# Kernel optimization log

Measured on AMD Instinct MI355X. Metric: run time of the kernel, lower is better.

The kernel has to match this reference:

```python
import jax, jax.numpy as jnp
import numpy as np

B = 8192
N_LAYERS = 2
NUM_PATCHES = 196  # 14*14
PATCH_OUT = 4
NUM_CLASSES = 10
IMG = 28


def setup_inputs() -> dict:
    key = jax.random.key(0)
    ks = jax.random.split(key, 5)
    x = jax.random.normal(ks[0], (B, 1, IMG, IMG), dtype=jnp.float32)
    ansatz_params = jax.random.normal(ks[1], (N_LAYERS, 4), dtype=jnp.float32)
    Wc = jax.random.normal(ks[2], (NUM_CLASSES, NUM_PATCHES * PATCH_OUT), dtype=jnp.float32) * 0.02
    bc = jnp.zeros((NUM_CLASSES,), jnp.float32)
    Wr = jax.random.normal(ks[3], (IMG * IMG, NUM_PATCHES * PATCH_OUT), dtype=jnp.float32) * 0.02
    br = jnp.zeros((IMG * IMG,), jnp.float32)
    return {"x": x, "ansatz_params": ansatz_params, "Wc": Wc, "bc": bc, "Wr": Wr, "br": br}


def _ry(state, theta, wire):
    # state: (N,2,2,2,2) real (RY and CNOT are real matrices).
    # RY(t) = [[cos(t/2), -sin(t/2)], [sin(t/2), cos(t/2)]]
    ax = wire + 1
    a0 = jnp.take(state, 0, axis=ax)
    a1 = jnp.take(state, 1, axis=ax)
    h = jnp.asarray(theta) * 0.5
    c, s = jnp.cos(h), jnp.sin(h)
    if c.ndim == 1:  # per-sample angle (N,)
        c = c[:, None, None, None]
        s = s[:, None, None, None]
    return jnp.stack([c * a0 - s * a1, s * a0 + c * a1], axis=ax)


def _cnot(state, ctrl, tgt):
    cax, tax = ctrl + 1, tgt + 1
    s0 = jnp.take(state, 0, axis=cax)
    s1 = jnp.take(state, 1, axis=cax)
    tax2 = tax - 1 if tax > cax else tax  # axis shift after removing ctrl axis
    s1 = jnp.flip(s1, axis=tax2)
    return jnp.stack([s0, s1], axis=cax)


def _simulate(patches_flat, params):
    # patches_flat: (N,4) encode angles; params: (L,4)
    N = patches_flat.shape[0]
    state = jnp.zeros((N, 2, 2, 2, 2), patches_flat.dtype).at[:, 0, 0, 0, 0].set(1.0)
    for w in range(4):
        state = _ry(state, patches_flat[:, w], w)
    for l in range(params.shape[0]):
        for w in range(4):
            state = _ry(state, params[l, w], w)
        for c, t in ((0, 1), (1, 2), (2, 3), (3, 0)):
            state = _cnot(state, c, t)
    p = state * state  # probabilities (real amplitudes)
    feats = jnp.stack(
        [jnp.sum(jnp.take(p, 0, axis=w + 1) - jnp.take(p, 1, axis=w + 1), axis=(1, 2, 3)) for w in range(4)],
        axis=-1,
    )  # (N,4) PauliZ expectations
    return feats


def reference(x, ansatz_params, Wc, bc, Wr, br):
    Bn = x.shape[0]
    # unfold(2,2,2).unfold(3,2,2) -> (B,1,14,14,2,2) -> (B,196,4)
    patches = x.reshape(Bn, 1, 14, 2, 14, 2).transpose(0, 1, 2, 4, 3, 5).reshape(Bn, NUM_PATCHES, 4)
    patches = patches / jnp.max(patches)
    feats = _simulate(patches.reshape(-1, 4), ansatz_params)  # (B*196, 4)
    flat = feats.reshape(Bn, NUM_PATCHES * PATCH_OUT)
    logits = flat @ Wc.T + bc
    recon = (flat @ Wr.T + br).reshape(Bn, 1, IMG, IMG)
    return jax.nn.log_softmax(logits, axis=-1), recon
```

## Files before the change

kernel.cpp:

```cpp
#include <hip/hip_runtime.h>
#include <hip/hip_bf16.h>

#define B_SZ   8192
#define NPATCH 196
#define FEAT   784
#define IMGPX  784
#define NCLS   10
#define NALL   794

typedef __attribute__((ext_vector_type(8))) short bf16x8;
typedef __attribute__((ext_vector_type(4))) float fx4;

__device__ inline unsigned f2ord(float f){
    unsigned u = __float_as_uint(f);
    return (u & 0x80000000u) ? ~u : (u | 0x80000000u);
}
__device__ inline float ord2f(unsigned u){
    return (u & 0x80000000u) ? __uint_as_float(u & 0x7FFFFFFFu)
                             : __uint_as_float(~u);
}
__device__ inline unsigned short f2bf(float f){
    union { __hip_bfloat16 h; unsigned short u; } cv;
    cv.h = __float2bfloat16(f);
    return cv.u;
}

__global__ __launch_bounds__(256) void k_max(const float* __restrict__ x,
                                             unsigned* __restrict__ maxslot){
    const int n4 = (B_SZ * IMGPX) / 4;
    float m = -3.0e38f;
    for (int i = blockIdx.x * 256 + threadIdx.x; i < n4; i += gridDim.x * 256){
        float4 v = ((const float4*)x)[i];
        m = fmaxf(m, fmaxf(fmaxf(v.x, v.y), fmaxf(v.z, v.w)));
    }
    #pragma unroll
    for (int off = 32; off > 0; off >>= 1)
        m = fmaxf(m, __shfl_down(m, off, 64));
    __shared__ float sm[4];
    int lane = threadIdx.x & 63, wv = threadIdx.x >> 6;
    if (lane == 0) sm[wv] = m;
    __syncthreads();
    if (threadIdx.x == 0){
        m = fmaxf(fmaxf(sm[0], sm[1]), fmaxf(sm[2], sm[3]));
        atomicMax(maxslot, f2ord(m));
    }
}

__global__ __launch_bounds__(256) void k_prep(const float* __restrict__ Wr,
                                              const float* __restrict__ Wc,
                                              const float* __restrict__ ansatz,
                                              unsigned short* __restrict__ Wall,
                                              float* __restrict__ trig){
    int t = blockIdx.x * 256 + threadIdx.x;
    if (blockIdx.x == 0 && threadIdx.x < 8){
        float p = ansatz[threadIdx.x];
        trig[threadIdx.x]     = cosf(0.5f * p);
        trig[8 + threadIdx.x] = sinf(0.5f * p);
    }
    const int nWr4  = (IMGPX * FEAT) / 4;
    const int nAll4 = (NALL  * FEAT) / 4;
    if (t < nAll4){
        float4 v = (t < nWr4) ? ((const float4*)Wr)[t]
                              : ((const float4*)Wc)[t - nWr4];
        ushort4 o;
        o.x = f2bf(v.x); o.y = f2bf(v.y); o.z = f2bf(v.z); o.w = f2bf(v.w);
        ((ushort4*)Wall)[t] = o;
    }
}

__global__ __launch_bounds__(256) void k_sim(const float* __restrict__ x,
                                             const unsigned* __restrict__ maxslot,
                                             const float* __restrict__ trig,
                                             unsigned short* __restrict__ flatb){
    int idx = blockIdx.x * 256 + threadIdx.x;
    if (idx >= B_SZ * NPATCH) return;
    int b  = idx / NPATCH;
    int p  = idx - b * NPATCH;
    int pi = p / 14;
    int pj = p - pi * 14;
    const float* base = x + b * IMGPX + pi * 2 * 28 + pj * 2;
    float2 r0 = *(const float2*)(base);
    float2 r1 = *(const float2*)(base + 28);
    float inv = 1.0f / ord2f(*maxslot);
    float th[4] = { r0.x * inv, r0.y * inv, r1.x * inv, r1.y * inv };
    float cw[4], sw[4];
    #pragma unroll
    for (int w = 0; w < 4; ++w) __sincosf(0.5f * th[w], &sw[w], &cw[w]);

    float a[16];
    a[0] = cw[0]; a[8] = sw[0];
    #pragma unroll
    for (int s = 0; s < 16; s += 8){ a[s + 4] = a[s] * sw[1]; a[s] *= cw[1]; }
    #pragma unroll
    for (int s = 0; s < 16; s += 4){ a[s + 2] = a[s] * sw[2]; a[s] *= cw[2]; }
    #pragma unroll
    for (int s = 0; s < 16; s += 2){ a[s + 1] = a[s] * sw[3]; a[s] *= cw[3]; }

    #pragma unroll
    for (int l = 0; l < 2; ++l){
        #pragma unroll
        for (int w = 0; w < 4; ++w){
            float cc = trig[l * 4 + w], ss = trig[8 + l * 4 + w];
            int msk = 8 >> w;
            #pragma unroll
            for (int st = 0; st < 16; ++st){
                if (!(st & msk)){
                    int s1 = st | msk;
                    float a0 = a[st], a1 = a[s1];
                    a[st] = cc * a0 - ss * a1;
                    a[s1] = ss * a0 + cc * a1;
                }
            }
        }
        #pragma unroll
        for (int ci = 0; ci < 4; ++ci){
            int cb = 8 >> ci;
            int tb = 8 >> ((ci + 1) & 3);
            #pragma unroll
            for (int st = 0; st < 16; ++st){
                if ((st & cb) && !(st & tb)){
                    int s1 = st | tb;
                    float tmp = a[st]; a[st] = a[s1]; a[s1] = tmp;
                }
            }
        }
    }
    float f0 = 0, f1 = 0, f2 = 0, f3 = 0;
    #pragma unroll
    for (int st = 0; st < 16; ++st){
        float pp = a[st] * a[st];
        f0 += (st & 8) ? -pp : pp;
        f1 += (st & 4) ? -pp : pp;
        f2 += (st & 2) ? -pp : pp;
        f3 += (st & 1) ? -pp : pp;
    }
    ushort4 o; o.x = f2bf(f0); o.y = f2bf(f1); o.z = f2bf(f2); o.w = f2bf(f3);
    ((ushort4*)flatb)[idx] = o;
}

__global__ __launch_bounds__(256) void k_gemm(const unsigned short* __restrict__ Aflat,
                                              const unsigned short* __restrict__ Wall,
                                              const float* __restrict__ br,
                                              const float* __restrict__ bc,
                                              float* __restrict__ recon,
                                              float* __restrict__ logits){
    __shared__ unsigned short As[64][40];
    __shared__ unsigned short Bs[64][40];
    const int t    = threadIdx.x;
    const int bm   = blockIdx.x, bn = blockIdx.y;
    const int lane = t & 63, wv = t >> 6;
    const int r    = lane & 15, q = lane >> 4;
    const int mb   = (wv >> 1) * 32, nb = (wv & 1) * 32;
    const int ldr  = t >> 2, kc = (t & 3) * 8;
    const int gm   = bm * 64 + ldr;
    const int gn   = bn * 64 + ldr;
    const bool bval = gn < NALL;

    fx4 acc[2][2] = {};

    for (int k0 = 0; k0 < FEAT; k0 += 32){
        int kk  = k0 + kc;
        bool kin = kk < FEAT;
        float4 av = {0, 0, 0, 0}, bv = {0, 0, 0, 0};
        if (kin)         av = *(const float4*)(Aflat + (size_t)gm * FEAT + kk);
        if (kin && bval) bv = *(const float4*)(Wall  + (size_t)gn * FEAT + kk);
        *(float4*)(&As[ldr][kc]) = av;
        *(float4*)(&Bs[ldr][kc]) = bv;
        __syncthreads();
        bf16x8 a0 = *(const bf16x8*)(&As[mb +      r][q * 8]);
        bf16x8 a1 = *(const bf16x8*)(&As[mb + 16 + r][q * 8]);
        bf16x8 b0 = *(const bf16x8*)(&Bs[nb +      r][q * 8]);
        bf16x8 b1 = *(const bf16x8*)(&Bs[nb + 16 + r][q * 8]);
        acc[0][0] = __builtin_amdgcn_mfma_f32_16x16x32_bf16(a0, b0, acc[0][0], 0, 0, 0);
        acc[0][1] = __builtin_amdgcn_mfma_f32_16x16x32_bf16(a0, b1, acc[0][1], 0, 0, 0);
        acc[1][0] = __builtin_amdgcn_mfma_f32_16x16x32_bf16(a1, b0, acc[1][0], 0, 0, 0);
        acc[1][1] = __builtin_amdgcn_mfma_f32_16x16x32_bf16(a1, b1, acc[1][1], 0, 0, 0);
        __syncthreads();
    }
    #pragma unroll
    for (int i = 0; i < 2; ++i)
        #pragma unroll
        for (int j = 0; j < 2; ++j)
            #pragma unroll
            for (int v = 0; v < 4; ++v){
                int m = bm * 64 + mb + i * 16 + q * 4 + v;
                int n = bn * 64 + nb + j * 16 + r;
                float val = acc[i][j][v];
                if (n < IMGPX)      recon[(size_t)m * IMGPX + n] = val + br[n];
                else if (n < NALL)  logits[m * NCLS + (n - IMGPX)] = val + bc[n - IMGPX];
            }
}

__global__ __launch_bounds__(256) void k_softmax(const float* __restrict__ logits,
                                                 float* __restrict__ out){
    int b = blockIdx.x * 256 + threadIdx.x;
    if (b >= B_SZ) return;
    float v[NCLS];
    float mx = -3.0e38f;
    #pragma unroll
    for (int c = 0; c < NCLS; ++c){ v[c] = logits[b * NCLS + c]; mx = fmaxf(mx, v[c]); }
    float s = 0.f;
    #pragma unroll
    for (int c = 0; c < NCLS; ++c) s += expf(v[c] - mx);
    float lse = mx + logf(s);
    #pragma unroll
    for (int c = 0; c < NCLS; ++c) out[b * NCLS + c] = v[c] - lse;
}

extern "C" void kernel_launch(void* const* d_in, const int* in_sizes, int n_in,
                              void* d_out, int out_size, void* d_ws, size_t ws_size,
                              hipStream_t stream){
    const float* x      = (const float*)d_in[0];
    const float* ansatz = (const float*)d_in[1];
    const float* Wc     = (const float*)d_in[2];
    const float* bc     = (const float*)d_in[3];
    const float* Wr     = (const float*)d_in[4];
    const float* br     = (const float*)d_in[5];
    float* out = (float*)d_out;

    unsigned char* ws = (unsigned char*)d_ws;
    unsigned*       maxslot = (unsigned*)ws;
    float*          trig    = (float*)(ws + 64);
    float*          logits  = (float*)(ws + 1024);
    unsigned short* Wall    = (unsigned short*)(ws + (1u << 19));
    unsigned short* flatb   = (unsigned short*)(ws + (1u << 21));

    hipMemsetAsync(maxslot, 0, 4, stream);
    k_max <<<1024, 256, 0, stream>>>(x, maxslot);
    k_prep<<<608,  256, 0, stream>>>(Wr, Wc, ansatz, Wall, trig);
    k_sim <<<(B_SZ * NPATCH + 255) / 256, 256, 0, stream>>>(x, maxslot, trig, flatb);
    dim3 g(128, 13);
    k_gemm<<<g, 256, 0, stream>>>(flatb, Wall, br, bc, out + B_SZ * NCLS, logits);
    k_softmax<<<32, 256, 0, stream>>>(logits, out);
}
```

Measured before the change: 148.5 us.

## Enlarge GEMM tiles with direct-to-LDS loads, fuse softmax and prep kernels

The GEMM moves from 64x64 to 128x128 block tiles, with a 4x4 MFMA accumulator grid per wave. Operands are padded to K=800 and N=896 so the loop needs no bounds checks, and global_load_lds writes them straight into shared memory. Log-softmax now runs in the epilogue of the last column block, and the max-reduction and weight-conversion kernels are merged into one launch, cutting two launches and the logits round-trip. The costs are higher register pressure, fewer blocks in flight (448), and some wasted work on zero padding.

```diff
diff --git a/kernel.cpp b/kernel.cpp
--- a/kernel.cpp
+++ b/kernel.cpp
@@ -4,9 +4,11 @@
 #define B_SZ   8192
 #define NPATCH 196
 #define FEAT   784
+#define KP     800
 #define IMGPX  784
 #define NCLS   10
 #define NALL   794
+#define NP     896
 
 typedef __attribute__((ext_vector_type(8))) short bf16x8;
 typedef __attribute__((ext_vector_type(4))) float fx4;
@@ -25,47 +27,50 @@
     return cv.u;
 }
 
-__global__ __launch_bounds__(256) void k_max(const float* __restrict__ x,
-                                             unsigned* __restrict__ maxslot){
-    const int n4 = (B_SZ * IMGPX) / 4;
-    float m = -3.0e38f;
-    for (int i = blockIdx.x * 256 + threadIdx.x; i < n4; i += gridDim.x * 256){
-        float4 v = ((const float4*)x)[i];
-        m = fmaxf(m, fmaxf(fmaxf(v.x, v.y), fmaxf(v.z, v.w)));
-    }
-    #pragma unroll
-    for (int off = 32; off > 0; off >>= 1)
-        m = fmaxf(m, __shfl_down(m, off, 64));
-    __shared__ float sm[4];
-    int lane = threadIdx.x & 63, wv = threadIdx.x >> 6;
-    if (lane == 0) sm[wv] = m;
-    __syncthreads();
-    if (threadIdx.x == 0){
-        m = fmaxf(fmaxf(sm[0], sm[1]), fmaxf(sm[2], sm[3]));
-        atomicMax(maxslot, f2ord(m));
-    }
-}
-
-__global__ __launch_bounds__(256) void k_prep(const float* __restrict__ Wr,
-                                              const float* __restrict__ Wc,
-                                              const float* __restrict__ ansatz,
-                                              unsigned short* __restrict__ Wall,
-                                              float* __restrict__ trig){
-    int t = blockIdx.x * 256 + threadIdx.x;
-    if (blockIdx.x == 0 && threadIdx.x < 8){
+__global__ __launch_bounds__(256) void k_maxprep(const float* __restrict__ x,
+                                                 const float* __restrict__ Wr,
+                                                 const float* __restrict__ Wc,
+                                                 const float* __restrict__ ansatz,
+                                                 unsigned* __restrict__ maxslot,
+                                                 unsigned short* __restrict__ Wall,
+                                                 float* __restrict__ trig){
+    if (blockIdx.x < 1024){
+        const int n4 = (B_SZ * IMGPX) / 4;
+        float m = -3.0e38f;
+        for (int i = blockIdx.x * 256 + threadIdx.x; i < n4; i += 1024 * 256){
+            float4 v = ((const float4*)x)[i];
+            m = fmaxf(m, fmaxf(fmaxf(v.x, v.y), fmaxf(v.z, v.w)));
+        }
+        #pragma unroll
+        for (int off = 32; off > 0; off >>= 1)
+            m = fmaxf(m, __shfl_down(m, off, 64));
+        __shared__ float sm[4];
+        int lane = threadIdx.x & 63, wv = threadIdx.x >> 6;
+        if (lane == 0) sm[wv] = m;
+        __syncthreads();
+        if (threadIdx.x == 0){
+            m = fmaxf(fmaxf(sm[0], sm[1]), fmaxf(sm[2], sm[3]));
+            atomicMax(maxslot, f2ord(m));
+        }
+        return;
+    }
+    if (blockIdx.x == 1024 && threadIdx.x < 8){
         float p = ansatz[threadIdx.x];
         trig[threadIdx.x]     = cosf(0.5f * p);
         trig[8 + threadIdx.x] = sinf(0.5f * p);
     }
-    const int nWr4  = (IMGPX * FEAT) / 4;
-    const int nAll4 = (NALL  * FEAT) / 4;
-    if (t < nAll4){
-        float4 v = (t < nWr4) ? ((const float4*)Wr)[t]
-                              : ((const float4*)Wc)[t - nWr4];
-        ushort4 o;
-        o.x = f2bf(v.x); o.y = f2bf(v.y); o.z = f2bf(v.z); o.w = f2bf(v.w);
-        ((ushort4*)Wall)[t] = o;
-    }
+    int e4  = (blockIdx.x - 1024) * 256 + threadIdx.x;
+    int row = e4 / 200;
+    int c4  = e4 - row * 200;
+    float4 v = {0.f, 0.f, 0.f, 0.f};
+    if (c4 < 196){
+        int col = c4 * 4;
+        if (row < IMGPX)       v = *(const float4*)(Wr + row * FEAT + col);
+        else if (row < NALL)   v = *(const float4*)(Wc + (row - IMGPX) * FEAT + col);
+    }
+    ushort4 o;
+    o.x = f2bf(v.x); o.y = f2bf(v.y); o.z = f2bf(v.z); o.w = f2bf(v.w);
+    ((ushort4*)Wall)[e4] = o;
 }
 
 __global__ __launch_bounds__(256) void k_sim(const float* __restrict__ x,
@@ -135,76 +140,104 @@
         f3 += (st & 1) ? -pp : pp;
     }
     ushort4 o; o.x = f2bf(f0); o.y = f2bf(f1); o.z = f2bf(f2); o.w = f2bf(f3);
-    ((ushort4*)flatb)[idx] = o;
-}
-
-__global__ __launch_bounds__(256) void k_gemm(const unsigned short* __restrict__ Aflat,
+    ((ushort4*)(flatb + (size_t)b * KP))[p] = o;
+    if (p < 4){
+        ushort4 z = {0, 0, 0, 0};
+        ((ushort4*)(flatb + (size_t)b * KP + FEAT))[p] = z;
+    }
+}
+
+__global__ __launch_bounds__(256) void k_gemm(const unsigned short* __restrict__ A,
                                               const unsigned short* __restrict__ Wall,
                                               const float* __restrict__ br,
                                               const float* __restrict__ bc,
                                               float* __restrict__ recon,
-                                              float* __restrict__ logits){
-    __shared__ unsigned short As[64][40];
-    __shared__ unsigned short Bs[64][40];
-    const int t    = threadIdx.x;
-    const int bm   = blockIdx.x, bn = blockIdx.y;
-    const int lane = t & 63, wv = t >> 6;
-    const int r    = lane & 15, q = lane >> 4;
-    const int mb   = (wv >> 1) * 32, nb = (wv & 1) * 32;
-    const int ldr  = t >> 2, kc = (t & 3) * 8;
-    const int gm   = bm * 64 + ldr;
-    const int gn   = bn * 64 + ldr;
-    const bool bval = gn < NALL;
-
-    fx4 acc[2][2] = {};
-
-    for (int k0 = 0; k0 < FEAT; k0 += 32){
-        int kk  = k0 + kc;
-        bool kin = kk < FEAT;
-        float4 av = {0, 0, 0, 0}, bv = {0, 0, 0, 0};
-        if (kin)         av = *(const float4*)(Aflat + (size_t)gm * FEAT + kk);
-        if (kin && bval) bv = *(const float4*)(Wall  + (size_t)gn * FEAT + kk);
-        *(float4*)(&As[ldr][kc]) = av;
-        *(float4*)(&Bs[ldr][kc]) = bv;
-        __syncthreads();
-        bf16x8 a0 = *(const bf16x8*)(&As[mb +      r][q * 8]);
-        bf16x8 a1 = *(const bf16x8*)(&As[mb + 16 + r][q * 8]);
-        bf16x8 b0 = *(const bf16x8*)(&Bs[nb +      r][q * 8]);
-        bf16x8 b1 = *(const bf16x8*)(&Bs[nb + 16 + r][q * 8]);
-        acc[0][0] = __builtin_amdgcn_mfma_f32_16x16x32_bf16(a0, b0, acc[0][0], 0, 0, 0);
-        acc[0][1] = __builtin_amdgcn_mfma_f32_16x16x32_bf16(a0, b1, acc[0][1], 0, 0, 0);
-        acc[1][0] = __builtin_amdgcn_mfma_f32_16x16x32_bf16(a1, b0, acc[1][0], 0, 0, 0);
-        acc[1][1] = __builtin_amdgcn_mfma_f32_16x16x32_bf16(a1, b1, acc[1][1], 0, 0, 0);
-        __syncthreads();
-    }
-    #pragma unroll
-    for (int i = 0; i < 2; ++i)
-        #pragma unroll
-        for (int j = 0; j < 2; ++j)
-            #pragma unroll
-            for (int v = 0; v < 4; ++v){
-                int m = bm * 64 + mb + i * 16 + q * 4 + v;
-                int n = bn * 64 + nb + j * 16 + r;
-                float val = acc[i][j][v];
-                if (n < IMGPX)      recon[(size_t)m * IMGPX + n] = val + br[n];
-                else if (n < NALL)  logits[m * NCLS + (n - IMGPX)] = val + bc[n - IMGPX];
+                                              float* __restrict__ outls){
+    __shared__ unsigned short As[128][32];
+    __shared__ unsigned short Bs[128][32];
+    __shared__ float sLg[128][NCLS];
+
+    const int t = threadIdx.x;
+    const int wv = t >> 6, lane = t & 63;
+    const int r = lane & 15, q = lane >> 4;
+    const int mb = (wv >> 1) * 64, nb = (wv & 1) * 64;
+    const int bm = blockIdx.x, bn = blockIdx.y;
+
+    const unsigned short* gptr[4];
+    const unsigned short* lptr[4];
+    #pragma unroll
+    for (int s = 0; s < 4; ++s){
+        int lin = s * 4 + wv;
+        int isB = lin >> 3;
+        int rb  = (lin & 7) * 16;
+        int row = rb + (lane >> 2);
+        int kc  = (lane & 3) * 8;
+        gptr[s] = (isB ? Wall + (size_t)(bn * 128 + row) * KP
+                       : A    + (size_t)(bm * 128 + row) * KP) + kc;
+        lptr[s] = isB ? &Bs[rb][0] : &As[rb][0];
+    }
+
+    fx4 acc[4][4] = {};
+
+    for (int k0 = 0; k0 < KP; k0 += 32){
+        #pragma unroll
+        for (int s = 0; s < 4; ++s){
+            __builtin_amdgcn_global_load_lds(
+                (const __attribute__((address_space(1))) unsigned int*)gptr[s],
+                (__attribute__((address_space(3))) unsigned int*)lptr[s],
+                16, 0, 0);
+            gptr[s] += 32;
+        }
+        __syncthreads();
+        bf16x8 af[4], bf[4];
+        #pragma unroll
+        for (int i = 0; i < 4; ++i) af[i] = *(const bf16x8*)&As[mb + i * 16 + r][q * 8];
+        #pragma unroll
+        for (int j = 0; j < 4; ++j) bf[j] = *(const bf16x8*)&Bs[nb + j * 16 + r][q * 8];
+        #pragma unroll
+        for (int i = 0; i < 4; ++i)
+            #pragma unroll
+            for (int j = 0; j < 4; ++j)
+                acc[i][j] = __builtin_amdgcn_mfma_f32_16x16x32_bf16(af[i], bf[j], acc[i][j], 0, 0, 0);
+        __syncthreads();
+    }
+
+    #pragma unroll
+    for (int i = 0; i < 4; ++i){
+        int ml = mb + i * 16 + q * 4;
+        int m  = bm * 128 + ml;
+        #pragma unroll
+        for (int j = 0; j < 4; ++j){
+            int n = bn * 128 + nb + j * 16 + r;
+            if (n < IMGPX){
+                float bias = br[n];
+                #pragma unroll
+                for (int v = 0; v < 4; ++v)
+                    recon[(size_t)(m + v) * IMGPX + n] = acc[i][j][v] + bias;
+            } else if (n < NALL){
+                float bias = bc[n - IMGPX];
+                #pragma unroll
+                for (int v = 0; v < 4; ++v)
+                    sLg[ml + v][n - IMGPX] = acc[i][j][v] + bias;
             }
-}
-
-__global__ __launch_bounds__(256) void k_softmax(const float* __restrict__ logits,
-                                                 float* __restrict__ out){
-    int b = blockIdx.x * 256 + threadIdx.x;
-    if (b >= B_SZ) return;
-    float v[NCLS];
-    float mx = -3.0e38f;
-    #pragma unroll
-    for (int c = 0; c < NCLS; ++c){ v[c] = logits[b * NCLS + c]; mx = fmaxf(mx, v[c]); }
-    float s = 0.f;
-    #pragma unroll
-    for (int c = 0; c < NCLS; ++c) s += expf(v[c] - mx);
-    float lse = mx + logf(s);
-    #pragma unroll
-    for (int c = 0; c < NCLS; ++c) out[b * NCLS + c] = v[c] - lse;
+        }
+    }
+    if (bn == 6){
+        __syncthreads();
+        if (t < 128){
+            float v[NCLS];
+            float mx = -3.0e38f;
+            #pragma unroll
+            for (int c = 0; c < NCLS; ++c){ v[c] = sLg[t][c]; mx = fmaxf(mx, v[c]); }
+            float s = 0.f;
+            #pragma unroll
+            for (int c = 0; c < NCLS; ++c) s += expf(v[c] - mx);
+            float lse = mx + logf(s);
+            size_t rowo = (size_t)(bm * 128 + t) * NCLS;
+            #pragma unroll
+            for (int c = 0; c < NCLS; ++c) outls[rowo + c] = v[c] - lse;
+        }
+    }
 }
 
 extern "C" void kernel_launch(void* const* d_in, const int* in_sizes, int n_in,
@@ -221,15 +254,12 @@
     unsigned char* ws = (unsigned char*)d_ws;
     unsigned*       maxslot = (unsigned*)ws;
     float*          trig    = (float*)(ws + 64);
-    float*          logits  = (float*)(ws + 1024);
-    unsigned short* Wall    = (unsigned short*)(ws + (1u << 19));
-    unsigned short* flatb   = (unsigned short*)(ws + (1u << 21));
+    unsigned short* flatb   = (unsigned short*)(ws + 4096);
+    unsigned short* Wall    = (unsigned short*)(ws + 4096 + (size_t)B_SZ * KP * 2);
 
     hipMemsetAsync(maxslot, 0, 4, stream);
-    k_max <<<1024, 256, 0, stream>>>(x, maxslot);
-    k_prep<<<608,  256, 0, stream>>>(Wr, Wc, ansatz, Wall, trig);
-    k_sim <<<(B_SZ * NPATCH + 255) / 256, 256, 0, stream>>>(x, maxslot, trig, flatb);
-    dim3 g(128, 13);
-    k_gemm<<<g, 256, 0, stream>>>(flatb, Wall, br, bc, out + B_SZ * NCLS, logits);
-    k_softmax<<<32, 256, 0, stream>>>(logits, out);
-}
+    k_maxprep<<<1724, 256, 0, stream>>>(x, Wr, Wc, ansatz, maxslot, Wall, trig);
+    k_sim<<<(B_SZ * NPATCH + 255) / 256, 256, 0, stream>>>(x, maxslot, trig, flatb);
+    dim3 g(64, 7);
+    k_gemm<<<g, 256, 0, stream>>>(flatb, Wall, br, bc, out + B_SZ * NCLS, out);
+}
```

Measured after the change: 144.0 us. 1.03x faster.
